# Kernel tuning notes

Hardware: AMD Instinct MI355X
Metric: run time of the kernel (lower is better)

## Reference

```python
import jax, jax.numpy as jnp
import numpy as np

D_OUT, D_IN, R, N_TOK = 4096, 4096, 16, 8192

def setup_inputs() -> dict:
    key = jax.random.key(0)
    k1, k2, k3, k4 = jax.random.split(key, 4)
    x = jax.random.normal(k1, (N_TOK, D_IN), dtype=jnp.float32)
    W = jax.random.normal(k2, (D_OUT, D_IN), dtype=jnp.float32) * (1.0 / np.sqrt(D_IN))
    bias = jax.random.normal(k3, (D_OUT,), dtype=jnp.float32) * 0.02
    lora_B = jnp.zeros((D_OUT, R), dtype=jnp.float32)  # torch init: zeros
    lora_A = jax.random.normal(k4, (R, D_IN), dtype=jnp.float32) / R  # torch init: randn / r
    lora_scale = jnp.float32(1.0)
    return {"x": x, "W": W, "bias": bias, "lora_B": lora_B, "lora_A": lora_A, "lora_scale": lora_scale}

def reference(x, W, bias, lora_B, lora_A, lora_scale):
    # Faithful to torch: weight = W + scale * B @ A; out = x @ weight.T + bias
    weight = W + lora_scale * (lora_B @ lora_A)  # [d_out, d_in]
    return jnp.einsum('ni,oi->no', x, weight) + bias
```

## Files before the change

kernel.cpp:

```cpp
#include <hip/hip_runtime.h>
#include <stdint.h>
#include <stddef.h>

#define M_TOK 8192
#define N_OUT 4096
#define K_IN  4096
#define R_LORA 16
#define BM 128
#define BN 256
#define BK 32

typedef __bf16 bf16_t;
typedef __bf16 bf16x4 __attribute__((ext_vector_type(4)));
typedef __bf16 bf16x8 __attribute__((ext_vector_type(8)));
typedef float floatx4 __attribute__((ext_vector_type(4)));

__device__ inline void async_copy16(const bf16_t* g, bf16_t* l) {
  __builtin_amdgcn_global_load_lds(
      (__attribute__((address_space(1))) void*)(uintptr_t)(const void*)g,
      (__attribute__((address_space(3))) void*)l,
      16, 0, 0);
}

__global__ __launch_bounds__(256) void cast_x_kernel(const float* __restrict__ x,
                                                     bf16_t* __restrict__ xb) {
  size_t i = (size_t)blockIdx.x * 256 + threadIdx.x;
  float4 a = ((const float4*)x)[i];
  bf16x4 v;
  v[0] = (bf16_t)a.x; v[1] = (bf16_t)a.y; v[2] = (bf16_t)a.z; v[3] = (bf16_t)a.w;
  *(bf16x4*)(xb + i * 4) = v;
}

__global__ __launch_bounds__(256) void make_weff(const float* __restrict__ W,
                                                 const float* __restrict__ lB,
                                                 const float* __restrict__ lA,
                                                 const float* __restrict__ scale_p,
                                                 bf16_t* __restrict__ wb) {
  const int o = blockIdx.x;
  __shared__ float Brow[R_LORA];
  if (threadIdx.x < R_LORA)
    Brow[threadIdx.x] = lB[(size_t)o * R_LORA + threadIdx.x] * (*scale_p);
  __syncthreads();
  const float4* W4 = (const float4*)(W + (size_t)o * K_IN);
  const float4* A4 = (const float4*)lA;
#pragma unroll
  for (int cc = 0; cc < 4; ++cc) {
    int idx = cc * 256 + (int)threadIdx.x;
    float4 w = W4[idx];
    float a0 = w.x, a1 = w.y, a2 = w.z, a3 = w.w;
#pragma unroll
    for (int r = 0; r < R_LORA; ++r) {
      float b = Brow[r];
      float4 av = A4[(size_t)r * (K_IN / 4) + idx];
      a0 += b * av.x; a1 += b * av.y; a2 += b * av.z; a3 += b * av.w;
    }
    bf16x4 v;
    v[0] = (bf16_t)a0; v[1] = (bf16_t)a1; v[2] = (bf16_t)a2; v[3] = (bf16_t)a3;
    *(bf16x4*)(wb + (size_t)o * K_IN + (size_t)idx * 4) = v;
  }
}

__global__ __launch_bounds__(256, 2) void gemm_bt(const bf16_t* __restrict__ A,
                                                  const bf16_t* __restrict__ Bw,
                                                  const float* __restrict__ bias,
                                                  float* __restrict__ C) {
  __shared__ bf16_t sA[BM * BK];
  __shared__ bf16_t sB[BN * BK];

  const int tid  = threadIdx.x;
  const int wave = tid >> 6;
  const int lane = tid & 63;
  const int lr   = lane & 15;
  const int quad = lane >> 4;
  const int bm = blockIdx.y * BM;
  const int bn = blockIdx.x * BN;
  const int wm = (wave >> 1) * 64;
  const int wn = (wave & 1) * 128;

  const bf16_t* gA[2];
  const bf16_t* gB[4];
  bf16_t* lA[2];
  bf16_t* lB[4];
#pragma unroll
  for (int i = 0; i < 2; ++i) {
    int s = i * 256 + wave * 64 + lane;
    int row = s >> 2;
    int q = ((s & 3) - (s >> 3)) & 3;
    gA[i] = A + (size_t)(bm + row) * K_IN + q * 8;
    lA[i] = sA + (size_t)(i * 256 + wave * 64) * 8;
  }
#pragma unroll
  for (int i = 0; i < 4; ++i) {
    int s = i * 256 + wave * 64 + lane;
    int row = s >> 2;
    int q = ((s & 3) - (s >> 3)) & 3;
    gB[i] = Bw + (size_t)(bn + row) * K_IN + q * 8;
    lB[i] = sB + (size_t)(i * 256 + wave * 64) * 8;
  }

  const int cofs = ((quad + (lr >> 1)) & 3) * 8;
  const bf16_t* fA[4];
  const bf16_t* fB[8];
#pragma unroll
  for (int i = 0; i < 4; ++i) fA[i] = sA + (wm + i * 16 + lr) * 32 + cofs;
#pragma unroll
  for (int j = 0; j < 8; ++j) fB[j] = sB + (wn + j * 16 + lr) * 32 + cofs;

  floatx4 acc[4][8];
#pragma unroll
  for (int i = 0; i < 4; ++i)
#pragma unroll
    for (int j = 0; j < 8; ++j) acc[i][j] = {0.f, 0.f, 0.f, 0.f};

  for (int k0 = 0; k0 < K_IN; k0 += BK) {
    __syncthreads();
    async_copy16(gA[0], lA[0]);
    async_copy16(gA[1], lA[1]);
    async_copy16(gB[0], lB[0]);
    async_copy16(gB[1], lB[1]);
    async_copy16(gB[2], lB[2]);
    async_copy16(gB[3], lB[3]);
    gA[0] += BK; gA[1] += BK;
    gB[0] += BK; gB[1] += BK; gB[2] += BK; gB[3] += BK;
    __syncthreads();

    bf16x8 a[4], b[8];
#pragma unroll
    for (int i = 0; i < 4; ++i) a[i] = *(const bf16x8*)fA[i];
#pragma unroll
    for (int j = 0; j < 8; ++j) b[j] = *(const bf16x8*)fB[j];
#pragma unroll
    for (int i = 0; i < 4; ++i)
#pragma unroll
      for (int j = 0; j < 8; ++j)
        acc[i][j] = __builtin_amdgcn_mfma_f32_16x16x32_bf16(a[i], b[j], acc[i][j], 0, 0, 0);
  }

#pragma unroll
  for (int j = 0; j < 8; ++j) {
    int col = bn + wn + j * 16 + lr;
    float bb = bias[col];
#pragma unroll
    for (int i = 0; i < 4; ++i) {
      int row0 = bm + wm + i * 16 + quad * 4;
      floatx4 v = acc[i][j];
#pragma unroll
      for (int r = 0; r < 4; ++r)
        C[(size_t)(row0 + r) * N_OUT + col] = v[r] + bb;
    }
  }
}

__global__ __launch_bounds__(256) void lora_xa(const float* __restrict__ x,
                                               const float* __restrict__ lA,
                                               const float* __restrict__ scale_p,
                                               float* __restrict__ t) {
  int m = blockIdx.x;
  int r = threadIdx.x & 15;
  int kcn = threadIdx.x >> 4;
  float acc = 0.f;
  const float* xr = x + (size_t)m * K_IN + kcn * 256;
  const float* ar = lA + (size_t)r * K_IN + kcn * 256;
  for (int k = 0; k < 256; k += 4) {
    float4 xv = *(const float4*)(xr + k);
    float4 av = *(const float4*)(ar + k);
    acc += xv.x * av.x + xv.y * av.y + xv.z * av.z + xv.w * av.w;
  }
  __shared__ float s[256];
  s[threadIdx.x] = acc;
  __syncthreads();
  if (threadIdx.x < 16) {
    float v = 0.f;
    for (int i = 0; i < 16; ++i) v += s[threadIdx.x + i * 16];
    t[(size_t)m * 16 + threadIdx.x] = v * (*scale_p);
  }
}

__global__ __launch_bounds__(256) void gemm_f32_fb(const float* __restrict__ X,
                                                   const float* __restrict__ W,
                                                   const float* __restrict__ bias,
                                                   const float* __restrict__ t,
                                                   const float* __restrict__ lB,
                                                   float* __restrict__ C) {
  __shared__ float sX[64][17];
  __shared__ float sW[64][17];
  int tid = threadIdx.x;
  int tx = tid & 15, ty = tid >> 4;
  int m0 = blockIdx.y * 64, n0 = blockIdx.x * 64;
  int lrow = tid >> 2, lcol = (tid & 3) * 4;
  float acc[4][4] = {};
  for (int k0 = 0; k0 < K_IN; k0 += 16) {
    __syncthreads();
    float4 xv = *(const float4*)(X + (size_t)(m0 + lrow) * K_IN + k0 + lcol);
    float4 wv = *(const float4*)(W + (size_t)(n0 + lrow) * K_IN + k0 + lcol);
    sX[lrow][lcol + 0] = xv.x; sX[lrow][lcol + 1] = xv.y;
    sX[lrow][lcol + 2] = xv.z; sX[lrow][lcol + 3] = xv.w;
    sW[lrow][lcol + 0] = wv.x; sW[lrow][lcol + 1] = wv.y;
    sW[lrow][lcol + 2] = wv.z; sW[lrow][lcol + 3] = wv.w;
    __syncthreads();
#pragma unroll
    for (int kk = 0; kk < 16; ++kk) {
      float xr[4], wr[4];
#pragma unroll
      for (int i = 0; i < 4; ++i) { xr[i] = sX[ty * 4 + i][kk]; wr[i] = sW[tx * 4 + i][kk]; }
#pragma unroll
      for (int i = 0; i < 4; ++i)
#pragma unroll
        for (int j = 0; j < 4; ++j) acc[i][j] += xr[i] * wr[j];
    }
  }
  for (int j = 0; j < 4; ++j) {
    int n = n0 + tx * 4 + j;
    float bb = bias[n];
    for (int i = 0; i < 4; ++i) {
      int m = m0 + ty * 4 + i;
      float l = 0.f;
      for (int r = 0; r < R_LORA; ++r) l += t[(size_t)m * 16 + r] * lB[(size_t)n * 16 + r];
      C[(size_t)m * N_OUT + n] = acc[i][j] + bb + l;
    }
  }
}

extern "C" void kernel_launch(void* const* d_in, const int* in_sizes, int n_in,
                              void* d_out, int out_size, void* d_ws, size_t ws_size,
                              hipStream_t stream) {
  const float* x     = (const float*)d_in[0];
  const float* W     = (const float*)d_in[1];
  const float* bias  = (const float*)d_in[2];
  const float* lB    = (const float*)d_in[3];
  const float* lA    = (const float*)d_in[4];
  const float* scale = (const float*)d_in[5];
  float* out = (float*)d_out;

  const size_t x_bytes = (size_t)M_TOK * K_IN * sizeof(bf16_t);
  const size_t w_bytes = (size_t)N_OUT * K_IN * sizeof(bf16_t);

  if (ws_size >= x_bytes + w_bytes) {
    bf16_t* xb = (bf16_t*)d_ws;
    bf16_t* wb = (bf16_t*)((char*)d_ws + x_bytes);
    cast_x_kernel<<<(M_TOK * K_IN / 4) / 256, 256, 0, stream>>>(x, xb);
    make_weff<<<N_OUT, 256, 0, stream>>>(W, lB, lA, scale, wb);
    gemm_bt<<<dim3(N_OUT / BN, M_TOK / BM), 256, 0, stream>>>(xb, wb, bias, out);
  } else {
    float* t = (float*)d_ws;
    lora_xa<<<M_TOK, 256, 0, stream>>>(x, lA, scale, t);
    gemm_f32_fb<<<dim3(N_OUT / 64, M_TOK / 64), 256, 0, stream>>>(x, W, bias, t, lB, out);
  }
}
```

Before: 561.8 us.

## Double-buffer GEMM LDS tiles and keep lora_A in registers in make_weff

The bf16 GEMM now uses two LDS buffers per operand and issues async global-to-LDS loads for the next K tile before running MFMAs on the current one, so memory latency can overlap with compute. The make_weff kernel is re-gridded so each thread holds a slice of lora_A in registers and reuses it across 32 output rows, instead of re-reading lora_A for every row. This doubles GEMM shared-memory use to about 48 KB per block, which may limit occupancy, and adds register pressure in make_weff.

```diff
diff --git a/kernel.cpp b/kernel.cpp
--- a/kernel.cpp
+++ b/kernel.cpp
@@ -36,27 +36,28 @@
                                                  const float* __restrict__ lA,
                                                  const float* __restrict__ scale_p,
                                                  bf16_t* __restrict__ wb) {
-  const int o = blockIdx.x;
-  __shared__ float Brow[R_LORA];
-  if (threadIdx.x < R_LORA)
-    Brow[threadIdx.x] = lB[(size_t)o * R_LORA + threadIdx.x] * (*scale_p);
-  __syncthreads();
-  const float4* W4 = (const float4*)(W + (size_t)o * K_IN);
-  const float4* A4 = (const float4*)lA;
-#pragma unroll
-  for (int cc = 0; cc < 4; ++cc) {
-    int idx = cc * 256 + (int)threadIdx.x;
-    float4 w = W4[idx];
+  const int kbase = blockIdx.x * 1024 + threadIdx.x * 4;
+  const int o0    = blockIdx.y * 32;
+  const float scale = *scale_p;
+
+  float4 areg[R_LORA];
+#pragma unroll
+  for (int r = 0; r < R_LORA; ++r)
+    areg[r] = *(const float4*)(lA + (size_t)r * K_IN + kbase);
+
+  for (int oo = 0; oo < 32; ++oo) {
+    const int o = o0 + oo;
+    float4 w = *(const float4*)(W + (size_t)o * K_IN + kbase);
     float a0 = w.x, a1 = w.y, a2 = w.z, a3 = w.w;
 #pragma unroll
     for (int r = 0; r < R_LORA; ++r) {
-      float b = Brow[r];
-      float4 av = A4[(size_t)r * (K_IN / 4) + idx];
-      a0 += b * av.x; a1 += b * av.y; a2 += b * av.z; a3 += b * av.w;
+      float b = lB[(size_t)o * R_LORA + r] * scale;
+      a0 += b * areg[r].x; a1 += b * areg[r].y;
+      a2 += b * areg[r].z; a3 += b * areg[r].w;
     }
     bf16x4 v;
     v[0] = (bf16_t)a0; v[1] = (bf16_t)a1; v[2] = (bf16_t)a2; v[3] = (bf16_t)a3;
-    *(bf16x4*)(wb + (size_t)o * K_IN + (size_t)idx * 4) = v;
+    *(bf16x4*)(wb + (size_t)o * K_IN + kbase) = v;
   }
 }
 
@@ -64,8 +65,8 @@
                                                   const bf16_t* __restrict__ Bw,
                                                   const float* __restrict__ bias,
                                                   float* __restrict__ C) {
-  __shared__ bf16_t sA[BM * BK];
-  __shared__ bf16_t sB[BN * BK];
+  __shared__ bf16_t sA[2 * BM * BK];
+  __shared__ bf16_t sB[2 * BN * BK];
 
   const int tid  = threadIdx.x;
   const int wave = tid >> 6;
@@ -79,15 +80,15 @@
 
   const bf16_t* gA[2];
   const bf16_t* gB[4];
-  bf16_t* lA[2];
-  bf16_t* lB[4];
+  bf16_t* lA0[2];
+  bf16_t* lB0[4];
 #pragma unroll
   for (int i = 0; i < 2; ++i) {
     int s = i * 256 + wave * 64 + lane;
     int row = s >> 2;
     int q = ((s & 3) - (s >> 3)) & 3;
     gA[i] = A + (size_t)(bm + row) * K_IN + q * 8;
-    lA[i] = sA + (size_t)(i * 256 + wave * 64) * 8;
+    lA0[i] = sA + (size_t)(i * 256 + wave * 64) * 8;
   }
 #pragma unroll
   for (int i = 0; i < 4; ++i) {
@@ -95,7 +96,7 @@
     int row = s >> 2;
     int q = ((s & 3) - (s >> 3)) & 3;
     gB[i] = Bw + (size_t)(bn + row) * K_IN + q * 8;
-    lB[i] = sB + (size_t)(i * 256 + wave * 64) * 8;
+    lB0[i] = sB + (size_t)(i * 256 + wave * 64) * 8;
   }
 
   const int cofs = ((quad + (lr >> 1)) & 3) * 8;
@@ -112,29 +113,42 @@
 #pragma unroll
     for (int j = 0; j < 8; ++j) acc[i][j] = {0.f, 0.f, 0.f, 0.f};
 
-  for (int k0 = 0; k0 < K_IN; k0 += BK) {
-    __syncthreads();
-    async_copy16(gA[0], lA[0]);
-    async_copy16(gA[1], lA[1]);
-    async_copy16(gB[0], lB[0]);
-    async_copy16(gB[1], lB[1]);
-    async_copy16(gB[2], lB[2]);
-    async_copy16(gB[3], lB[3]);
-    gA[0] += BK; gA[1] += BK;
-    gB[0] += BK; gB[1] += BK; gB[2] += BK; gB[3] += BK;
-    __syncthreads();
-
-    bf16x8 a[4], b[8];
-#pragma unroll
-    for (int i = 0; i < 4; ++i) a[i] = *(const bf16x8*)fA[i];
-#pragma unroll
-    for (int j = 0; j < 8; ++j) b[j] = *(const bf16x8*)fB[j];
-#pragma unroll
-    for (int i = 0; i < 4; ++i)
-#pragma unroll
-      for (int j = 0; j < 8; ++j)
-        acc[i][j] = __builtin_amdgcn_mfma_f32_16x16x32_bf16(a[i], b[j], acc[i][j], 0, 0, 0);
-  }
+#define STAGE(buf_ofsA, buf_ofsB)                                   \
+  do {                                                              \
+    async_copy16(gA[0], lA0[0] + (buf_ofsA));                       \
+    async_copy16(gA[1], lA0[1] + (buf_ofsA));                       \
+    async_copy16(gB[0], lB0[0] + (buf_ofsB));                       \
+    async_copy16(gB[1], lB0[1] + (buf_ofsB));                       \
+    async_copy16(gB[2], lB0[2] + (buf_ofsB));                       \
+    async_copy16(gB[3], lB0[3] + (buf_ofsB));                       \
+    gA[0] += BK; gA[1] += BK;                                       \
+    gB[0] += BK; gB[1] += BK; gB[2] += BK; gB[3] += BK;             \
+  } while (0)
+
+#define COMPUTE(buf_ofsA, buf_ofsB)                                                   \
+  do {                                                                                \
+    bf16x8 a[4], b[8];                                                                \
+    _Pragma("unroll") for (int i = 0; i < 4; ++i)                                     \
+        a[i] = *(const bf16x8*)(fA[i] + (buf_ofsA));                                  \
+    _Pragma("unroll") for (int j = 0; j < 8; ++j)                                     \
+        b[j] = *(const bf16x8*)(fB[j] + (buf_ofsB));                                  \
+    _Pragma("unroll") for (int i = 0; i < 4; ++i)                                     \
+        _Pragma("unroll") for (int j = 0; j < 8; ++j)                                 \
+            acc[i][j] = __builtin_amdgcn_mfma_f32_16x16x32_bf16(a[i], b[j],           \
+                                                                acc[i][j], 0, 0, 0); \
+  } while (0)
+
+  STAGE(0, 0);
+  for (int it = 0; it < K_IN / BK; it += 2) {
+    __syncthreads();
+    STAGE(BM * BK, BN * BK);
+    COMPUTE(0, 0);
+    __syncthreads();
+    if (it + 2 < K_IN / BK) STAGE(0, 0);
+    COMPUTE(BM * BK, BN * BK);
+  }
+#undef STAGE
+#undef COMPUTE
 
 #pragma unroll
   for (int j = 0; j < 8; ++j) {
@@ -239,7 +253,7 @@
     bf16_t* xb = (bf16_t*)d_ws;
     bf16_t* wb = (bf16_t*)((char*)d_ws + x_bytes);
     cast_x_kernel<<<(M_TOK * K_IN / 4) / 256, 256, 0, stream>>>(x, xb);
-    make_weff<<<N_OUT, 256, 0, stream>>>(W, lB, lA, scale, wb);
+    make_weff<<<dim3(K_IN / 1024, N_OUT / 32), 256, 0, stream>>>(W, lB, lA, scale, wb);
     gemm_bt<<<dim3(N_OUT / BN, M_TOK / BM), 256, 0, stream>>>(xb, wb, bias, out);
   } else {
     float* t = (float*)d_ws;
```

Measured after the change: 550.7 us. -2.0%, faster.
